# Performance work log

Measured on AMD Instinct MI355X. Metric: run time of the kernel, lower is better.

The kernel has to match this reference:

```python
import jax, jax.numpy as jnp
import numpy as np

SAMPLERATE = 22050
N_OCTAVES = 16
N_SAMPLES = 32768
MIN_FREQ = 20.0 / (SAMPLERATE // 2)
MAX_FREQ = 3000.0 / (SAMPLERATE // 2)
FREQ_RANGE = MAX_FREQ - MIN_FREQ
BASE_RESONANCE = 0.01


def max_norm(x, axis=-1, eps=1e-8):
    return x / (jnp.max(jnp.abs(x), axis=axis, keepdims=True) + eps)


def exponential_decay(decay_values, n_octaves):
    # decay_values: (B, E, 1). Note the original applies sigmoid here on top of
    # the sigmoid already applied in forward (sigmoid_decay=True) -> double sigmoid.
    dv = jax.nn.sigmoid(decay_values)  # (B, E, 1)
    resonance_factor = (1.0 - BASE_RESONANCE) * 0.99
    decay = BASE_RESONANCE + dv * resonance_factor  # (B, E, 1)
    logd = jnp.log(decay + 1e-12)
    b, e, _ = decay_values.shape
    # cumsum of a per-(b,e) constant over octaves, then exp (matches torch code;
    # F.interpolate to size==n_octaves is the identity here)
    logd = jnp.broadcast_to(logd, (b, e, n_octaves))
    return jnp.exp(jnp.cumsum(logd, axis=-1))  # (B, E, O)


def setup_inputs() -> dict:
    key = jax.random.key(0)
    k1, k2, k3 = jax.random.split(key, 3)
    B, E = 8, 64
    return {
        "f0": jax.random.uniform(k1, (B, E, 1), dtype=jnp.float32),
        "decay_coefficients": jax.random.normal(k2, (B, E, 1), dtype=jnp.float32),
        "unused": jnp.zeros((B, E, 1), dtype=jnp.float32),
        "freq_spacing": jax.random.uniform(k3, (B, E, 1), dtype=jnp.float32),
    }


def reference(f0, decay_coefficients, unused, freq_spacing):
    b, e, _ = f0.shape
    O, S = N_OCTAVES, N_SAMPLES

    f0 = jnp.abs(f0)  # (B, E, 1)
    # sigmoid_decay=True path: sigmoid applied before exponential_decay
    exp_decays = exponential_decay(jax.nn.sigmoid(decay_coefficients), O)  # (B, E, O)

    f0 = (MIN_FREQ + f0 * FREQ_RANGE) * jnp.pi  # (B, E, 1)

    # freq_spacing repeated over octaves then cumsum -> per-octave factors
    factors = jnp.cumsum(jnp.broadcast_to(freq_spacing, (b, e, O)), axis=-1)
    f0s = f0 * factors  # (B, E, O)

    # nyquist cutoff
    f0s = f0s * (f0s < 1.0)

    # phase: cumsum over samples of constant per-octave frequency (faithful to torch)
    phase = jnp.cumsum(jnp.broadcast_to(f0s[..., None], (b, e, O, S)), axis=-1)
    osc = jnp.sin(phase)  # (B, E, O, S)

    osc = osc * exp_decays[..., None]
    osc = jnp.sum(osc, axis=2)  # (B, E, S)
    return max_norm(osc, axis=-1)
```

## Files before the change

kernel.cpp:

```cpp
#include <hip/hip_runtime.h>
#include <math.h>

#define N_OCT 16
#define NS    32768
#define TPB   1024
#define SPT   (NS / TPB)
#define N_BE  512

typedef float v2f __attribute__((ext_vector_type(2)));

static __device__ __forceinline__ v2f fma2(v2f a, v2f b, v2f c) {
    return __builtin_elementwise_fma(a, b, c);
}

template<int NP>
static __device__ __forceinline__ void run_body(
    const int t,
    const double* __restrict__ sR, const float* __restrict__ sCH,
    const float* __restrict__ sCL, const float* __restrict__ sAMP,
    float* __restrict__ wmax, float* __restrict__ orow)
{
    v2f xp[NP], xc[NP], c2h[NP], c2l[NP];

    #pragma unroll
    for (int o = 0; o < 2 * NP; ++o) {
        const double r = sR[o];
        const float  a = sAMP[o];
        double p0 = r * (double)(t + 1);
        p0 -= floor(p0);
        double pm = r * (double)(t + 1 - TPB);
        pm -= floor(pm);
        float xcur  = a * __builtin_amdgcn_sinf((float)p0);
        float xprev = a * __builtin_amdgcn_sinf((float)pm);
        const int j = o >> 1;
        if ((o & 1) == 0) {
            xc[j].x = xcur;   xp[j].x = xprev;
            c2h[j].x = sCH[o]; c2l[j].x = sCL[o];
        } else {
            xc[j].y = xcur;   xp[j].y = xprev;
            c2h[j].y = sCH[o]; c2l[j].y = sCL[o];
        }
    }

    float lmax = 0.0f;
    #pragma unroll 4
    for (int k = 0; k < SPT; ++k) {
        v2f acc2 = (v2f)(0.0f);
        #pragma unroll
        for (int j = 0; j < NP; ++j) {
            acc2 += xc[j];
            v2f xn = fma2(c2h[j], xc[j], fma2(c2l[j], xc[j], -xp[j]));
            xp[j] = xc[j];
            xc[j] = xn;
        }
        lmax = fmaxf(lmax, fabsf(acc2.x + acc2.y));
    }

    #pragma unroll
    for (int off = 32; off > 0; off >>= 1)
        lmax = fmaxf(lmax, __shfl_down(lmax, off, 64));
    if ((t & 63) == 0) wmax[t >> 6] = lmax;
    __syncthreads();
    float bmax = wmax[0];
    #pragma unroll
    for (int w = 1; w < TPB / 64; ++w) bmax = fmaxf(bmax, wmax[w]);
    const float norm = 1.0f / (bmax + 1e-8f);

    v2f cur[NP], nxt[NP];
    #pragma unroll
    for (int j = 0; j < NP; ++j) {
        cur[j] = xp[j] * norm;
        nxt[j] = xc[j] * norm;
    }
    #pragma unroll 4
    for (int m = SPT - 1; m >= 0; --m) {
        v2f acc2 = (v2f)(0.0f);
        #pragma unroll
        for (int j = 0; j < NP; ++j) {
            acc2 += cur[j];
            v2f pv = fma2(c2h[j], cur[j], fma2(c2l[j], cur[j], -nxt[j]));
            nxt[j] = cur[j];
            cur[j] = pv;
        }
        orow[m * TPB + t] = acc2.x + acc2.y;
    }
}

__global__ __launch_bounds__(TPB, 1)
void f0res_kernel(const float* __restrict__ f0_in,
                  const float* __restrict__ dc_in,
                  const float* __restrict__ fs_in,
                  float* __restrict__ out)
{
    __shared__ double sR[N_OCT];
    __shared__ float  sCH[N_OCT], sCL[N_OCT], sAMP[N_OCT];
    __shared__ float  wmax[TPB / 64];
    __shared__ int    sLive;

    const int be = blockIdx.x;
    const int t  = threadIdx.x;

    if (t < N_OCT) {
        const int o = t;
        const float f0a = fabsf(f0_in[be]);
        const float dc  = dc_in[be];
        const float fs  = fs_in[be];

        const float MINF = (float)(20.0 / 11025.0);
        const float FRNG = (float)(3000.0 / 11025.0 - 20.0 / 11025.0);

        const float s1    = 1.0f / (1.0f + __expf(-dc));
        const float dv    = 1.0f / (1.0f + __expf(-s1));
        const float decay = 0.01f + dv * 0.9801f;
        const float logd  = __logf(decay + 1e-12f);
        const float f0r   = (MINF + f0a * FRNG) * 3.14159274101257324f;

        float cl = 0.f, cf = 0.f;
        for (int i = 0; i <= o; ++i) { cl += logd; cf += fs; }
        float ed  = __expf(cl);
        float f0s = f0r * cf;
        float a   = ed;
        const bool live = (f0s < 1.0f);
        if (!live) { a = 0.0f; f0s = 0.0f; }

        unsigned long long lm = __ballot(live);
        if (o == 0) sLive = __popcll(lm);

        const double inv2pi = 0.15915494309189535;
        double r = (double)f0s * inv2pi;

        double drev = r * (double)TPB;
        drev -= floor(drev);
        double c2d = 2.0 * cos(drev * 6.283185307179586);
        float  ch  = (float)c2d;

        sR[o]   = r;
        sCH[o]  = ch;
        sCL[o]  = (float)(c2d - (double)ch);
        sAMP[o] = a;
    }
    __syncthreads();

    const int NP = (sLive + 1) >> 1;
    float* __restrict__ orow = out + (size_t)be * NS;

    switch (NP) {
    case 0: {
        #pragma unroll
        for (int m = 0; m < SPT; ++m) orow[m * TPB + t] = 0.0f;
        break;
    }
    case 1: run_body<1>(t, sR, sCH, sCL, sAMP, wmax, orow); break;
    case 2: run_body<2>(t, sR, sCH, sCL, sAMP, wmax, orow); break;
    case 3: run_body<3>(t, sR, sCH, sCL, sAMP, wmax, orow); break;
    case 4: run_body<4>(t, sR, sCH, sCL, sAMP, wmax, orow); break;
    case 5: run_body<5>(t, sR, sCH, sCL, sAMP, wmax, orow); break;
    case 6: run_body<6>(t, sR, sCH, sCL, sAMP, wmax, orow); break;
    case 7: run_body<7>(t, sR, sCH, sCL, sAMP, wmax, orow); break;
    default: run_body<8>(t, sR, sCH, sCL, sAMP, wmax, orow); break;
    }
}

extern "C" void kernel_launch(void* const* d_in, const int* in_sizes, int n_in,
                              void* d_out, int out_size, void* d_ws, size_t ws_size,
                              hipStream_t stream) {
    const float* f0 = (const float*)d_in[0];
    const float* dc = (const float*)d_in[1];
    const float* fs = (const float*)d_in[3];
    float* out = (float*)d_out;
    (void)d_ws; (void)ws_size;

    hipLaunchKernelGGL(f0res_kernel, dim3(N_BE), dim3(TPB),
                       0, stream, f0, dc, fs, out);
}
```

Measured before the change: 108.7 us.

## Split each row across four blocks with two-kernel max then store pass

Each row of 32768 samples is now split into four chunks handled by separate 256-thread blocks, giving 2048 blocks instead of 512 blocks of 1024 threads. The first kernel runs the recurrence and writes per-chunk maxima to workspace; the second kernel seeds the oscillators again, reads the four maxima, and writes the normalized output forward. This trades one extra launch, a repeated constant setup and seeding step, and a workspace round-trip for finer-grained block scheduling and better occupancy across CUs.

```diff
diff --git a/kernel.cpp b/kernel.cpp
--- a/kernel.cpp
+++ b/kernel.cpp
@@ -1,11 +1,13 @@
 #include <hip/hip_runtime.h>
 #include <math.h>
 
-#define N_OCT 16
-#define NS    32768
-#define TPB   1024
-#define SPT   (NS / TPB)
-#define N_BE  512
+#define N_OCT  16
+#define NS     32768
+#define TPB    256
+#define NSPLIT 4
+#define CHUNK  (NS / NSPLIT)
+#define SPT    (CHUNK / TPB)
+#define N_BE   512
 
 typedef float v2f __attribute__((ext_vector_type(2)));
 
@@ -13,34 +15,92 @@
     return __builtin_elementwise_fma(a, b, c);
 }
 
+
+static __device__ __forceinline__ void make_consts(
+    int be, int t,
+    const float* __restrict__ f0_in, const float* __restrict__ dc_in,
+    const float* __restrict__ fs_in,
+    double* __restrict__ sR, float* __restrict__ sCH,
+    float* __restrict__ sCL, float* __restrict__ sAMP, int* __restrict__ sLive)
+{
+    if (t < N_OCT) {
+        const int o = t;
+        const float f0a = fabsf(f0_in[be]);
+        const float dc  = dc_in[be];
+        const float fs  = fs_in[be];
+
+        const float MINF = (float)(20.0 / 11025.0);
+        const float FRNG = (float)(3000.0 / 11025.0 - 20.0 / 11025.0);
+
+        const float s1    = 1.0f / (1.0f + __expf(-dc));
+        const float dv    = 1.0f / (1.0f + __expf(-s1));
+        const float decay = 0.01f + dv * 0.9801f;
+        const float logd  = __logf(decay + 1e-12f);
+        const float f0r   = (MINF + f0a * FRNG) * 3.14159274101257324f;
+
+        float cl = 0.f, cf = 0.f;
+        for (int i = 0; i <= o; ++i) { cl += logd; cf += fs; }
+        float ed  = __expf(cl);
+        float f0s = f0r * cf;
+        float a   = ed;
+        const bool live = (f0s < 1.0f);
+        if (!live) { a = 0.0f; f0s = 0.0f; }
+
+        unsigned long long lm = __ballot(live);
+        if (o == 0) *sLive = __popcll(lm);
+
+        const double inv2pi = 0.15915494309189535;
+        double r = (double)f0s * inv2pi;
+
+        double drev = r * (double)TPB;
+        drev -= floor(drev);
+        double c2d = 2.0 * cos(drev * 6.283185307179586);
+        float  ch  = (float)c2d;
+
+        sR[o]   = r;
+        sCH[o]  = ch;
+        sCL[o]  = (float)(c2d - (double)ch);
+        sAMP[o] = a;
+    }
+}
+
 template<int NP>
-static __device__ __forceinline__ void run_body(
-    const int t,
+static __device__ __forceinline__ void seed_state(
+    int base, int t,
     const double* __restrict__ sR, const float* __restrict__ sCH,
     const float* __restrict__ sCL, const float* __restrict__ sAMP,
-    float* __restrict__ wmax, float* __restrict__ orow)
-{
-    v2f xp[NP], xc[NP], c2h[NP], c2l[NP];
-
+    v2f* xp, v2f* xc, v2f* c2h, v2f* c2l)
+{
     #pragma unroll
     for (int o = 0; o < 2 * NP; ++o) {
         const double r = sR[o];
         const float  a = sAMP[o];
-        double p0 = r * (double)(t + 1);
+        double p0 = r * (double)(base + t + 1);
         p0 -= floor(p0);
-        double pm = r * (double)(t + 1 - TPB);
+        double pm = r * (double)(base + t + 1 - TPB);
         pm -= floor(pm);
         float xcur  = a * __builtin_amdgcn_sinf((float)p0);
         float xprev = a * __builtin_amdgcn_sinf((float)pm);
         const int j = o >> 1;
         if ((o & 1) == 0) {
-            xc[j].x = xcur;   xp[j].x = xprev;
+            xc[j].x = xcur;    xp[j].x = xprev;
             c2h[j].x = sCH[o]; c2l[j].x = sCL[o];
         } else {
-            xc[j].y = xcur;   xp[j].y = xprev;
+            xc[j].y = xcur;    xp[j].y = xprev;
             c2h[j].y = sCH[o]; c2l[j].y = sCL[o];
         }
     }
+}
+
+template<int NP>
+static __device__ __forceinline__ void body_max(
+    int base, int t,
+    const double* __restrict__ sR, const float* __restrict__ sCH,
+    const float* __restrict__ sCL, const float* __restrict__ sAMP,
+    float* __restrict__ wmax, float* __restrict__ slot)
+{
+    v2f xp[NP], xc[NP], c2h[NP], c2l[NP];
+    seed_state<NP>(base, t, sR, sCH, sCL, sAMP, xp, xc, c2h, c2l);
 
     float lmax = 0.0f;
     #pragma unroll 4
@@ -61,103 +121,118 @@
         lmax = fmaxf(lmax, __shfl_down(lmax, off, 64));
     if ((t & 63) == 0) wmax[t >> 6] = lmax;
     __syncthreads();
-    float bmax = wmax[0];
+    if (t == 0) {
+        float bmax = wmax[0];
+        #pragma unroll
+        for (int w = 1; w < TPB / 64; ++w) bmax = fmaxf(bmax, wmax[w]);
+        *slot = bmax;
+    }
+}
+
+template<int NP>
+static __device__ __forceinline__ void body_store(
+    int base, int t, float norm,
+    const double* __restrict__ sR, const float* __restrict__ sCH,
+    const float* __restrict__ sCL, const float* __restrict__ sAMP,
+    float* __restrict__ ochunk)
+{
+    v2f xp[NP], xc[NP], c2h[NP], c2l[NP];
+    seed_state<NP>(base, t, sR, sCH, sCL, sAMP, xp, xc, c2h, c2l);
     #pragma unroll
-    for (int w = 1; w < TPB / 64; ++w) bmax = fmaxf(bmax, wmax[w]);
-    const float norm = 1.0f / (bmax + 1e-8f);
-
-    v2f cur[NP], nxt[NP];
-    #pragma unroll
-    for (int j = 0; j < NP; ++j) {
-        cur[j] = xp[j] * norm;
-        nxt[j] = xc[j] * norm;
-    }
+    for (int j = 0; j < NP; ++j) { xc[j] *= norm; xp[j] *= norm; }
+
     #pragma unroll 4
-    for (int m = SPT - 1; m >= 0; --m) {
+    for (int k = 0; k < SPT; ++k) {
         v2f acc2 = (v2f)(0.0f);
         #pragma unroll
         for (int j = 0; j < NP; ++j) {
-            acc2 += cur[j];
-            v2f pv = fma2(c2h[j], cur[j], fma2(c2l[j], cur[j], -nxt[j]));
-            nxt[j] = cur[j];
-            cur[j] = pv;
+            acc2 += xc[j];
+            v2f xn = fma2(c2h[j], xc[j], fma2(c2l[j], xc[j], -xp[j]));
+            xp[j] = xc[j];
+            xc[j] = xn;
         }
-        orow[m * TPB + t] = acc2.x + acc2.y;
+        ochunk[k * TPB + t] = acc2.x + acc2.y;
     }
 }
 
 __global__ __launch_bounds__(TPB, 1)
-void f0res_kernel(const float* __restrict__ f0_in,
-                  const float* __restrict__ dc_in,
-                  const float* __restrict__ fs_in,
-                  float* __restrict__ out)
+void f0res_max(const float* __restrict__ f0_in,
+               const float* __restrict__ dc_in,
+               const float* __restrict__ fs_in,
+               float* __restrict__ ws)
 {
     __shared__ double sR[N_OCT];
     __shared__ float  sCH[N_OCT], sCL[N_OCT], sAMP[N_OCT];
     __shared__ float  wmax[TPB / 64];
     __shared__ int    sLive;
 
-    const int be = blockIdx.x;
-    const int t  = threadIdx.x;
-
-    if (t < N_OCT) {
-        const int o = t;
-        const float f0a = fabsf(f0_in[be]);
-        const float dc  = dc_in[be];
-        const float fs  = fs_in[be];
-
-        const float MINF = (float)(20.0 / 11025.0);
-        const float FRNG = (float)(3000.0 / 11025.0 - 20.0 / 11025.0);
-
-        const float s1    = 1.0f / (1.0f + __expf(-dc));
-        const float dv    = 1.0f / (1.0f + __expf(-s1));
-        const float decay = 0.01f + dv * 0.9801f;
-        const float logd  = __logf(decay + 1e-12f);
-        const float f0r   = (MINF + f0a * FRNG) * 3.14159274101257324f;
-
-        float cl = 0.f, cf = 0.f;
-        for (int i = 0; i <= o; ++i) { cl += logd; cf += fs; }
-        float ed  = __expf(cl);
-        float f0s = f0r * cf;
-        float a   = ed;
-        const bool live = (f0s < 1.0f);
-        if (!live) { a = 0.0f; f0s = 0.0f; }
-
-        unsigned long long lm = __ballot(live);
-        if (o == 0) sLive = __popcll(lm);
-
-        const double inv2pi = 0.15915494309189535;
-        double r = (double)f0s * inv2pi;
-
-        double drev = r * (double)TPB;
-        drev -= floor(drev);
-        double c2d = 2.0 * cos(drev * 6.283185307179586);
-        float  ch  = (float)c2d;
-
-        sR[o]   = r;
-        sCH[o]  = ch;
-        sCL[o]  = (float)(c2d - (double)ch);
-        sAMP[o] = a;
-    }
+    const int bid = blockIdx.x;
+    const int be  = bid >> 2;
+    const int q   = bid & 3;
+    const int t   = threadIdx.x;
+    const int base = q * CHUNK;
+
+    make_consts(be, t, f0_in, dc_in, fs_in, sR, sCH, sCL, sAMP, &sLive);
     __syncthreads();
 
     const int NP = (sLive + 1) >> 1;
-    float* __restrict__ orow = out + (size_t)be * NS;
+    float* slot = ws + bid;
+
+    switch (NP) {
+    case 0: if (t == 0) *slot = 0.0f; break;
+    case 1: body_max<1>(base, t, sR, sCH, sCL, sAMP, wmax, slot); break;
+    case 2: body_max<2>(base, t, sR, sCH, sCL, sAMP, wmax, slot); break;
+    case 3: body_max<3>(base, t, sR, sCH, sCL, sAMP, wmax, slot); break;
+    case 4: body_max<4>(base, t, sR, sCH, sCL, sAMP, wmax, slot); break;
+    case 5: body_max<5>(base, t, sR, sCH, sCL, sAMP, wmax, slot); break;
+    case 6: body_max<6>(base, t, sR, sCH, sCL, sAMP, wmax, slot); break;
+    case 7: body_max<7>(base, t, sR, sCH, sCL, sAMP, wmax, slot); break;
+    default: body_max<8>(base, t, sR, sCH, sCL, sAMP, wmax, slot); break;
+    }
+}
+
+__global__ __launch_bounds__(TPB, 1)
+void f0res_store(const float* __restrict__ f0_in,
+                 const float* __restrict__ dc_in,
+                 const float* __restrict__ fs_in,
+                 const float* __restrict__ ws,
+                 float* __restrict__ out)
+{
+    __shared__ double sR[N_OCT];
+    __shared__ float  sCH[N_OCT], sCL[N_OCT], sAMP[N_OCT];
+    __shared__ int    sLive;
+
+    const int bid = blockIdx.x;
+    const int be  = bid >> 2;
+    const int q   = bid & 3;
+    const int t   = threadIdx.x;
+    const int base = q * CHUNK;
+
+    make_consts(be, t, f0_in, dc_in, fs_in, sR, sCH, sCL, sAMP, &sLive);
+    __syncthreads();
+
+    const int r4 = be << 2;
+    const float bmax = fmaxf(fmaxf(ws[r4 + 0], ws[r4 + 1]),
+                             fmaxf(ws[r4 + 2], ws[r4 + 3]));
+    const float norm = 1.0f / (bmax + 1e-8f);
+
+    const int NP = (sLive + 1) >> 1;
+    float* __restrict__ ochunk = out + (size_t)be * NS + base;
 
     switch (NP) {
     case 0: {
         #pragma unroll
-        for (int m = 0; m < SPT; ++m) orow[m * TPB + t] = 0.0f;
+        for (int k = 0; k < SPT; ++k) ochunk[k * TPB + t] = 0.0f;
         break;
     }
-    case 1: run_body<1>(t, sR, sCH, sCL, sAMP, wmax, orow); break;
-    case 2: run_body<2>(t, sR, sCH, sCL, sAMP, wmax, orow); break;
-    case 3: run_body<3>(t, sR, sCH, sCL, sAMP, wmax, orow); break;
-    case 4: run_body<4>(t, sR, sCH, sCL, sAMP, wmax, orow); break;
-    case 5: run_body<5>(t, sR, sCH, sCL, sAMP, wmax, orow); break;
-    case 6: run_body<6>(t, sR, sCH, sCL, sAMP, wmax, orow); break;
-    case 7: run_body<7>(t, sR, sCH, sCL, sAMP, wmax, orow); break;
-    default: run_body<8>(t, sR, sCH, sCL, sAMP, wmax, orow); break;
+    case 1: body_store<1>(base, t, norm, sR, sCH, sCL, sAMP, ochunk); break;
+    case 2: body_store<2>(base, t, norm, sR, sCH, sCL, sAMP, ochunk); break;
+    case 3: body_store<3>(base, t, norm, sR, sCH, sCL, sAMP, ochunk); break;
+    case 4: body_store<4>(base, t, norm, sR, sCH, sCL, sAMP, ochunk); break;
+    case 5: body_store<5>(base, t, norm, sR, sCH, sCL, sAMP, ochunk); break;
+    case 6: body_store<6>(base, t, norm, sR, sCH, sCL, sAMP, ochunk); break;
+    case 7: body_store<7>(base, t, norm, sR, sCH, sCL, sAMP, ochunk); break;
+    default: body_store<8>(base, t, norm, sR, sCH, sCL, sAMP, ochunk); break;
     }
 }
 
@@ -168,8 +243,10 @@
     const float* dc = (const float*)d_in[1];
     const float* fs = (const float*)d_in[3];
     float* out = (float*)d_out;
-    (void)d_ws; (void)ws_size;
-
-    hipLaunchKernelGGL(f0res_kernel, dim3(N_BE), dim3(TPB),
-                       0, stream, f0, dc, fs, out);
-}
+    float* ws  = (float*)d_ws;
+
+    hipLaunchKernelGGL(f0res_max, dim3(N_BE * NSPLIT), dim3(TPB),
+                       0, stream, f0, dc, fs, ws);
+    hipLaunchKernelGGL(f0res_store, dim3(N_BE * NSPLIT), dim3(TPB),
+                       0, stream, f0, dc, fs, ws, out);
+}
```

Result: no change. 109.6 us (+0.9%).
